# Optimization experiments

Measured on AMD Instinct MI355X. Metric: run time of the kernel, lower is better.

The kernel has to match this reference:

```python
import jax, jax.numpy as jnp
import numpy as np

S, B, D = 2048, 2, 1024   # seq_len, batch, d_model
H, Dh = 16, 64            # n_head, d_head (H*Dh == D)
LN_EPS = 1e-5


def _rel_shift(x):
    # x: [qlen, klen, bsz, n_head] -- standard Transformer-XL relative shift
    q, k, b, n = x.shape
    x = jnp.pad(x, ((0, 0), (1, 0), (0, 0), (0, 0)))  # [q, k+1, b, n]
    x = x.reshape(k + 1, q, b, n)[1:]                  # drop first row
    return x.reshape(q, k, b, n)


def setup_inputs() -> dict:
    key = jax.random.key(0)
    ks = jax.random.split(key, 8)
    s = 0.02
    return {
        "x":    jax.random.normal(ks[0], (S, B, D), jnp.float32),
        "r":    jax.random.normal(ks[1], (1, D), jnp.float32),          # learned pos vector
        "rw":   jax.random.normal(ks[2], (H, Dh), jnp.float32),          # content bias
        "rr":   jax.random.normal(ks[3], (H, Dh), jnp.float32),          # position bias
        "ln_g": jnp.ones((D,), jnp.float32),
        "ln_b": jnp.zeros((D,), jnp.float32),
        "Wqkv": jax.random.normal(ks[4], (D, 3 * H * Dh), jnp.float32) * s,
        "Wr":   jax.random.normal(ks[5], (D, H * Dh), jnp.float32) * s,
        "Wo":   jax.random.normal(ks[6], (H * Dh, D), jnp.float32) * s,
    }


def reference(x, r, rw, rr, ln_g, ln_b, Wqkv, Wr, Wo):
    # Pre-LayerNorm (dropout = identity in eval mode)
    mu = jnp.mean(x, axis=-1, keepdims=True)
    var = jnp.mean(jnp.square(x - mu), axis=-1, keepdims=True)
    xn = (x - mu) * jax.lax.rsqrt(var + LN_EPS) * ln_g + ln_b   # [S,B,D]

    # relative position input: r expanded over seq
    r_exp = jnp.broadcast_to(r, (S, D))                          # [S,D]

    qkv = xn @ Wqkv                                              # [S,B,3*H*Dh]
    q, k, v = jnp.split(qkv, 3, axis=-1)
    q = q.reshape(S, B, H, Dh)
    k = k.reshape(S, B, H, Dh)
    v = v.reshape(S, B, H, Dh)
    rk = (r_exp @ Wr).reshape(S, H, Dh)                          # [S,H,Dh]

    scale = 1.0 / np.sqrt(Dh).astype(np.float32)
    AC = jnp.einsum('ibnd,jbnd->ijbn', q + rw, k)                # content term
    BD = jnp.einsum('ibnd,jnd->ijbn', q + rr, rk)                # position term
    BD = _rel_shift(BD)
    attn = jax.nn.softmax((AC + BD) * scale, axis=1)             # over key axis j

    av = jnp.einsum('ijbn,jbnd->ibnd', attn, v).reshape(S, B, H * Dh)
    return xn + av @ Wo                                          # residual w/ normed input
```

## Files before the change

### kernel.cpp

```cpp
#include <hip/hip_runtime.h>

typedef unsigned short u16;
typedef __attribute__((ext_vector_type(8))) __bf16 bf16x8;
typedef __attribute__((ext_vector_type(8))) u16 u16x8;
typedef __attribute__((ext_vector_type(4))) float f32x4;

__device__ __forceinline__ float bf2f(u16 u){
  union { unsigned int i; float f; } v; v.i = ((unsigned int)u) << 16; return v.f;
}
__device__ __forceinline__ u16 f2bf(float f){
  union { float f; unsigned int u; } v; v.f = f;
  unsigned int u = v.u;
  u += 0x7FFFu + ((u >> 16) & 1u);
  return (u16)(u >> 16);
}
__device__ __forceinline__ unsigned fbits(float f){
  union { float f; unsigned u; } v; v.f = f; return v.u;
}
__device__ __forceinline__ void gld_lds16(const u16* g, u16* l){
  __builtin_amdgcn_global_load_lds((const __attribute__((address_space(1))) unsigned int*)g,
                                   (__attribute__((address_space(3))) unsigned int*)l, 16, 0, 0);
}

__global__ __launch_bounds__(256) void transpose_k(const float* __restrict__ in, u16* __restrict__ out,
                                                   int R, int C){
  __shared__ float tile[32][33];
  const int bx = blockIdx.x * 32, by = blockIdx.y * 32;
  const int tx = threadIdx.x, ty = threadIdx.y;
  #pragma unroll
  for(int i = 0; i < 32; i += 8)
    tile[ty + i][tx] = in[(size_t)(by + ty + i) * C + bx + tx];
  __syncthreads();
  #pragma unroll
  for(int i = 0; i < 32; i += 8)
    out[(size_t)(bx + ty + i) * R + by + tx] = f2bf(tile[tx][ty + i]);
}

__global__ __launch_bounds__(256) void ln_k(const float* __restrict__ x, const float* __restrict__ gw,
                                            const float* __restrict__ bw, u16* __restrict__ xnb){
  const int row = blockIdx.x, t = threadIdx.x;
  const float* xr = x + (size_t)row * 1024;
  float4 xv = *reinterpret_cast<const float4*>(xr + t * 4);
  float s  = xv.x + xv.y + xv.z + xv.w;
  float s2 = xv.x*xv.x + xv.y*xv.y + xv.z*xv.z + xv.w*xv.w;
  #pragma unroll
  for(int m = 1; m <= 32; m <<= 1){ s += __shfl_xor(s, m, 64); s2 += __shfl_xor(s2, m, 64); }
  __shared__ float red[8];
  const int w = t >> 6, lane = t & 63;
  if(lane == 0){ red[w] = s; red[4 + w] = s2; }
  __syncthreads();
  float S1 = red[0] + red[1] + red[2] + red[3];
  float S2 = red[4] + red[5] + red[6] + red[7];
  float mu = S1 * (1.f/1024.f);
  float var = S2 * (1.f/1024.f) - mu * mu;
  float rstd = rsqrtf(var + 1e-5f);
  float4 gv = *reinterpret_cast<const float4*>(gw + t * 4);
  float4 bv = *reinterpret_cast<const float4*>(bw + t * 4);
  ushort4 o;
  o.x = f2bf((xv.x - mu) * rstd * gv.x + bv.x);
  o.y = f2bf((xv.y - mu) * rstd * gv.y + bv.y);
  o.z = f2bf((xv.z - mu) * rstd * gv.z + bv.z);
  o.w = f2bf((xv.w - mu) * rstd * gv.w + bv.w);
  *reinterpret_cast<ushort4*>(xnb + (size_t)row * 1024 + t * 4) = o;
}

__global__ __launch_bounds__(256) void rk0_k(const float* __restrict__ r, const float* __restrict__ Wr,
                                             float* __restrict__ rk0){
  const int n = blockIdx.x * 256 + threadIdx.x;
  const int d0 = blockIdx.y * 128;
  float acc = 0.f;
  for(int d = d0; d < d0 + 128; ++d)
    acc += r[d] * Wr[(size_t)d * 1024 + n];
  atomicAdd(&rk0[n], acc);
}

__global__ __launch_bounds__(256) void c_k(const u16* __restrict__ qk, const float* __restrict__ rr,
                                           const float* __restrict__ rk0, float* __restrict__ cc){
  const int w = threadIdx.x >> 6, lane = threadIdx.x & 63;
  const int ib = blockIdx.x * 4 + w;
  const u16* qp = qk + (size_t)ib * 2048 + lane * 16;
  u16x8 q0 = *reinterpret_cast<const u16x8*>(qp);
  u16x8 q1 = *reinterpret_cast<const u16x8*>(qp + 8);
  const float* rrp = rr + lane * 16;
  const float* rkp = rk0 + lane * 16;
  float s = 0.f;
  #pragma unroll
  for(int e = 0; e < 8; ++e){
    s += (bf2f(q0[e]) + rrp[e]) * rkp[e];
    s += (bf2f(q1[e]) + rrp[8 + e]) * rkp[8 + e];
  }
  s += __shfl_xor(s, 1, 64);
  s += __shfl_xor(s, 2, 64);
  if((lane & 3) == 0) cc[(size_t)ib * 16 + (lane >> 2)] = s;
}

__global__ __launch_bounds__(256) void vtrans_k(const u16* __restrict__ vnat, u16* __restrict__ vT){
  __shared__ u16 tl[128][40];
  const int t = threadIdx.x;
  const int i0 = blockIdx.x * 128, c0 = blockIdx.y * 32, b = blockIdx.z;
  {
    const int ii = t & 127, cs = (t >> 7) * 16;
    const u16* p = vnat + (size_t)((i0 + ii) * 2 + b) * 1024 + c0 + cs;
    *reinterpret_cast<u16x8*>(&tl[ii][cs])     = *reinterpret_cast<const u16x8*>(p);
    *reinterpret_cast<u16x8*>(&tl[ii][cs + 8]) = *reinterpret_cast<const u16x8*>(p + 8);
  }
  __syncthreads();
  const int dr = t & 31, seg = t >> 5;
  const int R = (b * 16 + (c0 >> 6)) * 64 + (c0 & 63) + dr;
  u16 tmp[16];
  #pragma unroll
  for(int e = 0; e < 16; ++e) tmp[e] = tl[seg * 16 + e][dr];
  u16* op = vT + (size_t)R * 2048 + i0 + seg * 16;
  *reinterpret_cast<u16x8*>(op)     = *reinterpret_cast<u16x8*>(&tmp[0]);
  *reinterpret_cast<u16x8*>(op + 8) = *reinterpret_cast<u16x8*>(&tmp[8]);
}

template<int MODE>
__global__ __launch_bounds__(256) void gemm_bt_k(const u16* __restrict__ A, const u16* __restrict__ BT,
                                                 const u16* __restrict__ res, u16* __restrict__ Cb,
                                                 float* __restrict__ Cf, u16* __restrict__ vnat,
                                                 int M, int N, int K){
  __shared__ u16 sA[128 * 32];
  __shared__ u16 sB[128 * 32];
  const int t = threadIdx.x;
  const int row0 = blockIdx.y * 128, col0 = blockIdx.x * 128;
  const int w = t >> 6, lane = t & 63, g = lane >> 4, lq = lane & 15;
  const int wr = (w >> 1) * 64, wc = (w & 1) * 64;
  const int s0 = t, s1 = t + 256;
  f32x4 zero4 = {0.f, 0.f, 0.f, 0.f};
  f32x4 acc[4][4];
  #pragma unroll
  for(int mi = 0; mi < 4; ++mi)
    #pragma unroll
    for(int ni = 0; ni < 4; ++ni) acc[mi][ni] = zero4;

  for(int kt = 0; kt < K; kt += 32){
    gld_lds16(A  + (size_t)(row0 + (s0 >> 2)) * K + kt + (s0 & 3) * 8, &sA[w * 512]);
    gld_lds16(A  + (size_t)(row0 + (s1 >> 2)) * K + kt + (s1 & 3) * 8, &sA[2048 + w * 512]);
    gld_lds16(BT + (size_t)(col0 + (s0 >> 2)) * K + kt + (s0 & 3) * 8, &sB[w * 512]);
    gld_lds16(BT + (size_t)(col0 + (s1 >> 2)) * K + kt + (s1 & 3) * 8, &sB[2048 + w * 512]);
    __syncthreads();
    bf16x8 af[4];
    #pragma unroll
    for(int mi = 0; mi < 4; ++mi)
      af[mi] = *reinterpret_cast<const bf16x8*>(&sA[(wr + mi * 16 + lq) * 32 + g * 8]);
    #pragma unroll
    for(int ni = 0; ni < 4; ++ni){
      bf16x8 bfr = *reinterpret_cast<const bf16x8*>(&sB[(wc + ni * 16 + lq) * 32 + g * 8]);
      #pragma unroll
      for(int mi = 0; mi < 4; ++mi)
        acc[mi][ni] = __builtin_amdgcn_mfma_f32_16x16x32_bf16(af[mi], bfr, acc[mi][ni], 0, 0, 0);
    }
    __syncthreads();
  }
  #pragma unroll
  for(int mi = 0; mi < 4; ++mi)
    #pragma unroll
    for(int ni = 0; ni < 4; ++ni)
      #pragma unroll
      for(int rg = 0; rg < 4; ++rg){
        const int row = row0 + wr + mi * 16 + g * 4 + rg;
        const int col = col0 + wc + ni * 16 + lq;
        float v = acc[mi][ni][rg];
        if(MODE == 1){
          v += bf2f(res[(size_t)row * N + col]);
          Cf[(size_t)row * N + col] = v;
        } else {
          if(col < 2048) Cb[(size_t)row * 2048 + col] = f2bf(v);
          else           vnat[(size_t)row * 1024 + (col - 2048)] = f2bf(v);
        }
      }
}

__global__ __launch_bounds__(256) void attn_k(const u16* __restrict__ qk, const u16* __restrict__ vT,
                                              const float* __restrict__ rw, const float* __restrict__ cc,
                                              u16* __restrict__ av){
  constexpr int S = 2048;
  __shared__ u16 ks[2][64 * 72];
  __shared__ u16 vs[2][64 * 72];
  __shared__ u16 ps[4][16 * 72];
  const int t = threadIdx.x;
  const int i0 = blockIdx.x * 64;
  const int bh = blockIdx.y;
  const int b = bh >> 4, h = bh & 15;
  const int w = t >> 6, lane = t & 63, g = lane >> 4, lq = lane & 15;
  const int iw0 = i0 + w * 16;
  const int i_lane = iw0 + lq;
  const float scale = 0.125f;
  const float L2E = 1.4426950408889634f;

  bf16x8 aq0, aq1;
  {
    const u16* qp = qk + (size_t)(i_lane * 2 + b) * 2048 + h * 64;
    u16x8 q0 = *reinterpret_cast<const u16x8*>(qp + g * 8);
    u16x8 q1 = *reinterpret_cast<const u16x8*>(qp + 32 + g * 8);
    const float* rwp = rw + h * 64 + g * 8;
    u16x8 a0, a1;
    #pragma unroll
    for(int e = 0; e < 8; ++e){
      a0[e] = f2bf((bf2f(q0[e]) + rwp[e]) * scale);
      a1[e] = f2bf((bf2f(q1[e]) + rwp[32 + e]) * scale);
    }
    aq0 = *reinterpret_cast<bf16x8*>(&a0);
    aq1 = *reinterpret_cast<bf16x8*>(&a1);
  }
  const float ciL = cc[(size_t)(i_lane * 2 + b) * 16 + h] * scale * L2E;
  const float cpL = (i_lane + 1 < S) ? cc[(size_t)((i_lane + 1) * 2 + b) * 16 + h] * scale * L2E : 0.0f;

  f32x4 zero4 = {0.f, 0.f, 0.f, 0.f};
  f32x4 acc[4], acc5 = zero4;
  #pragma unroll
  for(int ni = 0; ni < 4; ++ni) acc[ni] = zero4;
  bf16x8 ones;
  {
    u16x8 ob;
    #pragma unroll
    for(int e = 0; e < 8; ++e) ob[e] = 0x3F80;
    ones = *reinterpret_cast<bf16x8*>(&ob);
  }

  const int jr = t >> 2, c0 = (t & 3) * 16;
  {
    const u16* kp = qk + (size_t)(jr * 2 + b) * 2048 + 1024 + h * 64 + c0;
    *reinterpret_cast<u16x8*>(&ks[0][jr * 72 + c0])     = *reinterpret_cast<const u16x8*>(kp);
    *reinterpret_cast<u16x8*>(&ks[0][jr * 72 + c0 + 8]) = *reinterpret_cast<const u16x8*>(kp + 8);
    const u16* vp = vT + ((size_t)bh * 64 + jr) * 2048 + c0;
    *reinterpret_cast<u16x8*>(&vs[0][jr * 72 + c0])     = *reinterpret_cast<const u16x8*>(vp);
    *reinterpret_cast<u16x8*>(&vs[0][jr * 72 + c0 + 8]) = *reinterpret_cast<const u16x8*>(vp + 8);
  }
  __syncthreads();

  for(int n = 0; n < 32; ++n){
    const int p = n & 1;
    u16x8 k0, k1, v0, v1;
    const bool pre = (n + 1 < 32);
    if(pre){
      const int j0n = (n + 1) * 64;
      const u16* kp = qk + (size_t)((j0n + jr) * 2 + b) * 2048 + 1024 + h * 64 + c0;
      k0 = *reinterpret_cast<const u16x8*>(kp);
      k1 = *reinterpret_cast<const u16x8*>(kp + 8);
      const u16* vp = vT + ((size_t)bh * 64 + jr) * 2048 + j0n + c0;
      v0 = *reinterpret_cast<const u16x8*>(vp);
      v1 = *reinterpret_cast<const u16x8*>(vp + 8);
    }
    const int j0 = n * 64;
    const bool below = (j0 + 63 <= iw0);
    const bool above = (j0 >= iw0 + 17);
    #pragma unroll
    for(int jt = 0; jt < 4; ++jt){
      f32x4 s4 = zero4;
      bf16x8 b0 = *reinterpret_cast<const bf16x8*>(&ks[p][(jt * 16 + lq) * 72 + g * 8]);
      s4 = __builtin_amdgcn_mfma_f32_16x16x32_bf16(b0, aq0, s4, 0, 0, 0);
      bf16x8 b1 = *reinterpret_cast<const bf16x8*>(&ks[p][(jt * 16 + lq) * 72 + 32 + g * 8]);
      s4 = __builtin_amdgcn_mfma_f32_16x16x32_bf16(b1, aq1, s4, 0, 0, 0);
      float pv[4];
      if(below){
        #pragma unroll
        for(int rg = 0; rg < 4; ++rg)
          pv[rg] = __builtin_amdgcn_exp2f(fmaf(s4[rg], L2E, ciL));
      } else if(above){
        #pragma unroll
        for(int rg = 0; rg < 4; ++rg)
          pv[rg] = __builtin_amdgcn_exp2f(fmaf(s4[rg], L2E, cpL));
      } else {
        #pragma unroll
        for(int rg = 0; rg < 4; ++rg){
          const int j = j0 + jt * 16 + g * 4 + rg;
          const float t1 = (j <= i_lane) ? ciL : cpL;
          const float bdL = (j == i_lane + 1) ? 0.0f : t1;
          pv[rg] = __builtin_amdgcn_exp2f(fmaf(s4[rg], L2E, bdL));
        }
      }
      uint2 pk;
      pk.x = __builtin_amdgcn_perm(fbits(pv[1]), fbits(pv[0]), 0x07060302);
      pk.y = __builtin_amdgcn_perm(fbits(pv[3]), fbits(pv[2]), 0x07060302);
      *reinterpret_cast<uint2*>(&ps[w][lq * 72 + jt * 16 + g * 4]) = pk;
    }
    __asm__ __volatile__("s_waitcnt lgkmcnt(0)" ::: "memory");
    bf16x8 ap0 = *reinterpret_cast<const bf16x8*>(&ps[w][lq * 72 + g * 8]);
    bf16x8 ap1 = *reinterpret_cast<const bf16x8*>(&ps[w][lq * 72 + 32 + g * 8]);
    #pragma unroll
    for(int ni = 0; ni < 4; ++ni){
      bf16x8 bv0 = *reinterpret_cast<const bf16x8*>(&vs[p][(ni * 16 + lq) * 72 + g * 8]);
      acc[ni] = __builtin_amdgcn_mfma_f32_16x16x32_bf16(bv0, ap0, acc[ni], 0, 0, 0);
      bf16x8 bv1 = *reinterpret_cast<const bf16x8*>(&vs[p][(ni * 16 + lq) * 72 + 32 + g * 8]);
      acc[ni] = __builtin_amdgcn_mfma_f32_16x16x32_bf16(bv1, ap1, acc[ni], 0, 0, 0);
    }
    acc5 = __builtin_amdgcn_mfma_f32_16x16x32_bf16(ones, ap0, acc5, 0, 0, 0);
    acc5 = __builtin_amdgcn_mfma_f32_16x16x32_bf16(ones, ap1, acc5, 0, 0, 0);
    if(pre){
      const int q2 = p ^ 1;
      *reinterpret_cast<u16x8*>(&ks[q2][jr * 72 + c0])     = k0;
      *reinterpret_cast<u16x8*>(&ks[q2][jr * 72 + c0 + 8]) = k1;
      *reinterpret_cast<u16x8*>(&vs[q2][jr * 72 + c0])     = v0;
      *reinterpret_cast<u16x8*>(&vs[q2][jr * 72 + c0 + 8]) = v1;
    }
    __syncthreads();
  }
  const float rinv = 1.0f / acc5[0];
  #pragma unroll
  for(int ni = 0; ni < 4; ++ni){
    ushort4 o;
    o.x = f2bf(acc[ni][0] * rinv);
    o.y = f2bf(acc[ni][1] * rinv);
    o.z = f2bf(acc[ni][2] * rinv);
    o.w = f2bf(acc[ni][3] * rinv);
    const int d = ni * 16 + g * 4;
    *reinterpret_cast<ushort4*>(av + (size_t)(i_lane * 2 + b) * 1024 + h * 64 + d) = o;
  }
}

extern "C" void kernel_launch(void* const* d_in, const int* in_sizes, int n_in,
                              void* d_out, int out_size, void* d_ws, size_t ws_size,
                              hipStream_t stream){
  (void)in_sizes; (void)n_in; (void)out_size; (void)ws_size;
  const float* x    = (const float*)d_in[0];
  const float* r    = (const float*)d_in[1];
  const float* rw   = (const float*)d_in[2];
  const float* rr   = (const float*)d_in[3];
  const float* ln_g = (const float*)d_in[4];
  const float* ln_b = (const float*)d_in[5];
  const float* Wqkv = (const float*)d_in[6];
  const float* Wr   = (const float*)d_in[7];
  const float* Wo   = (const float*)d_in[8];
  char* ws = (char*)d_ws;
  u16*   xnb   = (u16*)(ws + 0);
  u16*   qk    = (u16*)(ws + 8388608);
  u16*   av    = (u16*)(ws + 25165824);
  u16*   woT   = (u16*)(ws + 33554432);
  u16*   wqkvT = (u16*)(ws + 35651584);
  u16*   vT    = (u16*)(ws + 41943040);
  float* rk0   = (float*)(ws + 50331648);
  float* cc    = (float*)(ws + 50335744);
  u16*   vnat  = av;
  float* out   = (float*)d_out;

  transpose_k<<<dim3(96, 32), dim3(32, 8), 0, stream>>>(Wqkv, wqkvT, 1024, 3072);
  transpose_k<<<dim3(32, 32), dim3(32, 8), 0, stream>>>(Wo, woT, 1024, 1024);
  ln_k<<<4096, 256, 0, stream>>>(x, ln_g, ln_b, xnb);
  hipMemsetAsync(rk0, 0, 4096, stream);
  rk0_k<<<dim3(4, 8), 256, 0, stream>>>(r, Wr, rk0);
  gemm_bt_k<2><<<dim3(24, 32), 256, 0, stream>>>(xnb, wqkvT, nullptr, qk, nullptr, vnat, 4096, 3072, 1024);
  vtrans_k<<<dim3(16, 32, 2), 256, 0, stream>>>(vnat, vT);
  c_k<<<1024, 256, 0, stream>>>(qk, rr, rk0, cc);
  attn_k<<<dim3(32, 32), 256, 0, stream>>>(qk, vT, rw, cc, av);
  gemm_bt_k<1><<<dim3(8, 32), 256, 0, stream>>>(av, woT, xnb, nullptr, out, nullptr, 4096, 1024, 1024);
}
```

Before: 253.9 us.

## Switch attention to 32x32x16 MFMA with register-resident P and 128-row query tiles

The attention kernel now uses 32x32x16 bf16 MFMA tiles, and each wave handles 32 query rows, so a block covers 128 queries and the grid shrinks by half. The P matrix stays in registers and is rearranged into the B-operand layout with cross-half lane shuffles, removing the LDS round trip for P. The row sum is accumulated in scalar registers instead of through a ones-vector MFMA. The LDS stride changes to 74 to avoid bank conflicts. This doubles K/V reuse per block and cuts LDS traffic, but raises register pressure and leaves only 512 blocks on the device.

```diff
diff --git a/kernel.cpp b/kernel.cpp
--- a/kernel.cpp
+++ b/kernel.cpp
@@ -4,6 +4,7 @@
 typedef __attribute__((ext_vector_type(8))) __bf16 bf16x8;
 typedef __attribute__((ext_vector_type(8))) u16 u16x8;
 typedef __attribute__((ext_vector_type(4))) float f32x4;
+typedef __attribute__((ext_vector_type(16))) float f32x16;
 
 __device__ __forceinline__ float bf2f(u16 u){
   union { unsigned int i; float f; } v; v.i = ((unsigned int)u) << 16; return v.f;
@@ -175,58 +176,49 @@
 __global__ __launch_bounds__(256) void attn_k(const u16* __restrict__ qk, const u16* __restrict__ vT,
                                               const float* __restrict__ rw, const float* __restrict__ cc,
                                               u16* __restrict__ av){
-  constexpr int S = 2048;
-  __shared__ u16 ks[2][64 * 72];
-  __shared__ u16 vs[2][64 * 72];
-  __shared__ u16 ps[4][16 * 72];
+  constexpr int S = 2048, ST = 74;
+  __shared__ u16 ks[2][64 * ST];
+  __shared__ u16 vs[2][64 * ST];
   const int t = threadIdx.x;
-  const int i0 = blockIdx.x * 64;
+  const int i0 = blockIdx.x * 128;
   const int bh = blockIdx.y;
   const int b = bh >> 4, h = bh & 15;
-  const int w = t >> 6, lane = t & 63, g = lane >> 4, lq = lane & 15;
-  const int iw0 = i0 + w * 16;
-  const int i_lane = iw0 + lq;
-  const float scale = 0.125f;
-  const float L2E = 1.4426950408889634f;
-
-  bf16x8 aq0, aq1;
+  const int w = t >> 6, lane = t & 63, m = lane & 31, q5 = lane >> 5;
+  const int iw0 = i0 + w * 32;
+  const int i_lane = iw0 + m;
+  const float SC = 0.125f * 1.4426950408889634f;
+
+  bf16x8 qf[4];
   {
     const u16* qp = qk + (size_t)(i_lane * 2 + b) * 2048 + h * 64;
-    u16x8 q0 = *reinterpret_cast<const u16x8*>(qp + g * 8);
-    u16x8 q1 = *reinterpret_cast<const u16x8*>(qp + 32 + g * 8);
-    const float* rwp = rw + h * 64 + g * 8;
-    u16x8 a0, a1;
-    #pragma unroll
-    for(int e = 0; e < 8; ++e){
-      a0[e] = f2bf((bf2f(q0[e]) + rwp[e]) * scale);
-      a1[e] = f2bf((bf2f(q1[e]) + rwp[32 + e]) * scale);
-    }
-    aq0 = *reinterpret_cast<bf16x8*>(&a0);
-    aq1 = *reinterpret_cast<bf16x8*>(&a1);
-  }
-  const float ciL = cc[(size_t)(i_lane * 2 + b) * 16 + h] * scale * L2E;
-  const float cpL = (i_lane + 1 < S) ? cc[(size_t)((i_lane + 1) * 2 + b) * 16 + h] * scale * L2E : 0.0f;
-
-  f32x4 zero4 = {0.f, 0.f, 0.f, 0.f};
-  f32x4 acc[4], acc5 = zero4;
-  #pragma unroll
-  for(int ni = 0; ni < 4; ++ni) acc[ni] = zero4;
-  bf16x8 ones;
-  {
-    u16x8 ob;
-    #pragma unroll
-    for(int e = 0; e < 8; ++e) ob[e] = 0x3F80;
-    ones = *reinterpret_cast<bf16x8*>(&ob);
-  }
+    const float* rwp = rw + h * 64;
+    #pragma unroll
+    for(int kt = 0; kt < 4; ++kt){
+      const int dbase = kt * 16 + q5 * 8;
+      u16x8 qv = *reinterpret_cast<const u16x8*>(qp + dbase);
+      u16x8 a;
+      #pragma unroll
+      for(int e = 0; e < 8; ++e) a[e] = f2bf((bf2f(qv[e]) + rwp[dbase + e]) * SC);
+      qf[kt] = *reinterpret_cast<bf16x8*>(&a);
+    }
+  }
+  const float ciL = cc[(size_t)(i_lane * 2 + b) * 16 + h] * SC;
+  const float cpL = (i_lane + 1 < S) ? cc[(size_t)((i_lane + 1) * 2 + b) * 16 + h] * SC : 0.0f;
+
+  f32x16 acc0, acc1, z16;
+  #pragma unroll
+  for(int e = 0; e < 16; ++e) z16[e] = 0.f;
+  acc0 = z16; acc1 = z16;
+  float rsum = 0.f;
 
   const int jr = t >> 2, c0 = (t & 3) * 16;
   {
     const u16* kp = qk + (size_t)(jr * 2 + b) * 2048 + 1024 + h * 64 + c0;
-    *reinterpret_cast<u16x8*>(&ks[0][jr * 72 + c0])     = *reinterpret_cast<const u16x8*>(kp);
-    *reinterpret_cast<u16x8*>(&ks[0][jr * 72 + c0 + 8]) = *reinterpret_cast<const u16x8*>(kp + 8);
+    *reinterpret_cast<u16x8*>(&ks[0][jr * ST + c0])     = *reinterpret_cast<const u16x8*>(kp);
+    *reinterpret_cast<u16x8*>(&ks[0][jr * ST + c0 + 8]) = *reinterpret_cast<const u16x8*>(kp + 8);
     const u16* vp = vT + ((size_t)bh * 64 + jr) * 2048 + c0;
-    *reinterpret_cast<u16x8*>(&vs[0][jr * 72 + c0])     = *reinterpret_cast<const u16x8*>(vp);
-    *reinterpret_cast<u16x8*>(&vs[0][jr * 72 + c0 + 8]) = *reinterpret_cast<const u16x8*>(vp + 8);
+    *reinterpret_cast<u16x8*>(&vs[0][jr * ST + c0])     = *reinterpret_cast<const u16x8*>(vp);
+    *reinterpret_cast<u16x8*>(&vs[0][jr * ST + c0 + 8]) = *reinterpret_cast<const u16x8*>(vp + 8);
   }
   __syncthreads();
 
@@ -244,69 +236,89 @@
       v1 = *reinterpret_cast<const u16x8*>(vp + 8);
     }
     const int j0 = n * 64;
-    const bool below = (j0 + 63 <= iw0);
-    const bool above = (j0 >= iw0 + 17);
-    #pragma unroll
-    for(int jt = 0; jt < 4; ++jt){
-      f32x4 s4 = zero4;
-      bf16x8 b0 = *reinterpret_cast<const bf16x8*>(&ks[p][(jt * 16 + lq) * 72 + g * 8]);
-      s4 = __builtin_amdgcn_mfma_f32_16x16x32_bf16(b0, aq0, s4, 0, 0, 0);
-      bf16x8 b1 = *reinterpret_cast<const bf16x8*>(&ks[p][(jt * 16 + lq) * 72 + 32 + g * 8]);
-      s4 = __builtin_amdgcn_mfma_f32_16x16x32_bf16(b1, aq1, s4, 0, 0, 0);
-      float pv[4];
-      if(below){
+    bf16x8 pfrag[4];
+    #pragma unroll
+    for(int jt = 0; jt < 2; ++jt){
+      const int tj0 = j0 + jt * 32;
+      f32x16 s = z16;
+      #pragma unroll
+      for(int kt = 0; kt < 4; ++kt){
+        bf16x8 ka = *reinterpret_cast<const bf16x8*>(&ks[p][(jt * 32 + m) * ST + kt * 16 + q5 * 8]);
+        s = __builtin_amdgcn_mfma_f32_32x32x16_bf16(ka, qf[kt], s, 0, 0, 0);
+      }
+      float pv[16];
+      if(tj0 + 31 <= iw0){
         #pragma unroll
-        for(int rg = 0; rg < 4; ++rg)
-          pv[rg] = __builtin_amdgcn_exp2f(fmaf(s4[rg], L2E, ciL));
-      } else if(above){
+        for(int r = 0; r < 16; ++r) pv[r] = __builtin_amdgcn_exp2f(s[r] + ciL);
+      } else if(tj0 >= iw0 + 33){
         #pragma unroll
-        for(int rg = 0; rg < 4; ++rg)
-          pv[rg] = __builtin_amdgcn_exp2f(fmaf(s4[rg], L2E, cpL));
+        for(int r = 0; r < 16; ++r) pv[r] = __builtin_amdgcn_exp2f(s[r] + cpL);
       } else {
         #pragma unroll
-        for(int rg = 0; rg < 4; ++rg){
-          const int j = j0 + jt * 16 + g * 4 + rg;
+        for(int r = 0; r < 16; ++r){
+          const int j = tj0 + (r & 3) + 8 * (r >> 2) + 4 * q5;
           const float t1 = (j <= i_lane) ? ciL : cpL;
           const float bdL = (j == i_lane + 1) ? 0.0f : t1;
-          pv[rg] = __builtin_amdgcn_exp2f(fmaf(s4[rg], L2E, bdL));
+          pv[r] = __builtin_amdgcn_exp2f(s[r] + bdL);
         }
       }
-      uint2 pk;
-      pk.x = __builtin_amdgcn_perm(fbits(pv[1]), fbits(pv[0]), 0x07060302);
-      pk.y = __builtin_amdgcn_perm(fbits(pv[3]), fbits(pv[2]), 0x07060302);
-      *reinterpret_cast<uint2*>(&ps[w][lq * 72 + jt * 16 + g * 4]) = pk;
-    }
-    __asm__ __volatile__("s_waitcnt lgkmcnt(0)" ::: "memory");
-    bf16x8 ap0 = *reinterpret_cast<const bf16x8*>(&ps[w][lq * 72 + g * 8]);
-    bf16x8 ap1 = *reinterpret_cast<const bf16x8*>(&ps[w][lq * 72 + 32 + g * 8]);
-    #pragma unroll
-    for(int ni = 0; ni < 4; ++ni){
-      bf16x8 bv0 = *reinterpret_cast<const bf16x8*>(&vs[p][(ni * 16 + lq) * 72 + g * 8]);
-      acc[ni] = __builtin_amdgcn_mfma_f32_16x16x32_bf16(bv0, ap0, acc[ni], 0, 0, 0);
-      bf16x8 bv1 = *reinterpret_cast<const bf16x8*>(&vs[p][(ni * 16 + lq) * 72 + 32 + g * 8]);
-      acc[ni] = __builtin_amdgcn_mfma_f32_16x16x32_bf16(bv1, ap1, acc[ni], 0, 0, 0);
-    }
-    acc5 = __builtin_amdgcn_mfma_f32_16x16x32_bf16(ones, ap0, acc5, 0, 0, 0);
-    acc5 = __builtin_amdgcn_mfma_f32_16x16x32_bf16(ones, ap1, acc5, 0, 0, 0);
+      #pragma unroll
+      for(int r = 0; r < 16; ++r) rsum += pv[r];
+      unsigned pk[8];
+      #pragma unroll
+      for(int q = 0; q < 8; ++q)
+        pk[q] = __builtin_amdgcn_perm(fbits(pv[2 * q + 1]), fbits(pv[2 * q]), 0x07060302);
+      unsigned sAx = (q5 == 0) ? pk[2] : pk[0];
+      unsigned sAy = (q5 == 0) ? pk[3] : pk[1];
+      unsigned rAx = (unsigned)__shfl_xor((int)sAx, 32, 64);
+      unsigned rAy = (unsigned)__shfl_xor((int)sAy, 32, 64);
+      unsigned sBx = (q5 == 0) ? pk[6] : pk[4];
+      unsigned sBy = (q5 == 0) ? pk[7] : pk[5];
+      unsigned rBx = (unsigned)__shfl_xor((int)sBx, 32, 64);
+      unsigned rBy = (unsigned)__shfl_xor((int)sBy, 32, 64);
+      union { unsigned u[4]; bf16x8 bf; } f0, f1;
+      if(q5 == 0){
+        f0.u[0] = pk[0]; f0.u[1] = pk[1]; f0.u[2] = rAx; f0.u[3] = rAy;
+        f1.u[0] = pk[4]; f1.u[1] = pk[5]; f1.u[2] = rBx; f1.u[3] = rBy;
+      } else {
+        f0.u[0] = rAx; f0.u[1] = rAy; f0.u[2] = pk[2]; f0.u[3] = pk[3];
+        f1.u[0] = rBx; f1.u[1] = rBy; f1.u[2] = pk[6]; f1.u[3] = pk[7];
+      }
+      pfrag[jt * 2 + 0] = f0.bf;
+      pfrag[jt * 2 + 1] = f1.bf;
+    }
+    #pragma unroll
+    for(int kt = 0; kt < 4; ++kt){
+      bf16x8 va0 = *reinterpret_cast<const bf16x8*>(&vs[p][(m) * ST + kt * 16 + q5 * 8]);
+      acc0 = __builtin_amdgcn_mfma_f32_32x32x16_bf16(va0, pfrag[kt], acc0, 0, 0, 0);
+      bf16x8 va1 = *reinterpret_cast<const bf16x8*>(&vs[p][(32 + m) * ST + kt * 16 + q5 * 8]);
+      acc1 = __builtin_amdgcn_mfma_f32_32x32x16_bf16(va1, pfrag[kt], acc1, 0, 0, 0);
+    }
     if(pre){
       const int q2 = p ^ 1;
-      *reinterpret_cast<u16x8*>(&ks[q2][jr * 72 + c0])     = k0;
-      *reinterpret_cast<u16x8*>(&ks[q2][jr * 72 + c0 + 8]) = k1;
-      *reinterpret_cast<u16x8*>(&vs[q2][jr * 72 + c0])     = v0;
-      *reinterpret_cast<u16x8*>(&vs[q2][jr * 72 + c0 + 8]) = v1;
+      *reinterpret_cast<u16x8*>(&ks[q2][jr * ST + c0])     = k0;
+      *reinterpret_cast<u16x8*>(&ks[q2][jr * ST + c0 + 8]) = k1;
+      *reinterpret_cast<u16x8*>(&vs[q2][jr * ST + c0])     = v0;
+      *reinterpret_cast<u16x8*>(&vs[q2][jr * ST + c0 + 8]) = v1;
     }
     __syncthreads();
   }
-  const float rinv = 1.0f / acc5[0];
-  #pragma unroll
-  for(int ni = 0; ni < 4; ++ni){
-    ushort4 o;
-    o.x = f2bf(acc[ni][0] * rinv);
-    o.y = f2bf(acc[ni][1] * rinv);
-    o.z = f2bf(acc[ni][2] * rinv);
-    o.w = f2bf(acc[ni][3] * rinv);
-    const int d = ni * 16 + g * 4;
-    *reinterpret_cast<ushort4*>(av + (size_t)(i_lane * 2 + b) * 1024 + h * 64 + d) = o;
+  rsum += __shfl_xor(rsum, 32, 64);
+  const float rinv = 1.0f / rsum;
+  u16* op = av + (size_t)(i_lane * 2 + b) * 1024 + h * 64;
+  #pragma unroll
+  for(int dt = 0; dt < 2; ++dt){
+    const f32x16& A = dt ? acc1 : acc0;
+    #pragma unroll
+    for(int rq = 0; rq < 4; ++rq){
+      ushort4 o;
+      o.x = f2bf(A[rq * 4 + 0] * rinv);
+      o.y = f2bf(A[rq * 4 + 1] * rinv);
+      o.z = f2bf(A[rq * 4 + 2] * rinv);
+      o.w = f2bf(A[rq * 4 + 3] * rinv);
+      const int d0 = dt * 32 + 8 * rq + 4 * q5;
+      *reinterpret_cast<ushort4*>(op + d0) = o;
+    }
   }
 }
 
@@ -343,6 +355,6 @@
   gemm_bt_k<2><<<dim3(24, 32), 256, 0, stream>>>(xnb, wqkvT, nullptr, qk, nullptr, vnat, 4096, 3072, 1024);
   vtrans_k<<<dim3(16, 32, 2), 256, 0, stream>>>(vnat, vT);
   c_k<<<1024, 256, 0, stream>>>(qk, rr, rk0, cc);
-  attn_k<<<dim3(32, 32), 256, 0, stream>>>(qk, vT, rw, cc, av);
+  attn_k<<<dim3(16, 32), 256, 0, stream>>>(qk, vT, rw, cc, av);
   gemm_bt_k<1><<<dim3(8, 32), 256, 0, stream>>>(av, woT, xnb, nullptr, out, nullptr, 4096, 1024, 1024);
 }
```

Measured after the change: 236.0 us. 7.0% less time.
